# Optimization experiments

Measured on AMD Instinct MI355X. Metric: run time of the kernel, lower is better.

Reference implementation:

```python
import jax, jax.numpy as jnp
import numpy as np

DIM = 768      # embedding dim
NH = 12        # num heads
HD = DIM // NH # head dim = 64
WIN = 14       # window size
MLP = 4 * DIM  # mlp hidden
EPS = 1e-5     # torch LayerNorm default


def _layernorm(x, g, b):
    m = x.mean(-1, keepdims=True)
    v = ((x - m) ** 2).mean(-1, keepdims=True)
    return (x - m) * jax.lax.rsqrt(v + EPS) * g + b


def setup_inputs() -> dict:
    key = jax.random.key(0)
    ks = jax.random.split(key, 8)
    def n(k, shape, s=0.02):
        return jax.random.normal(k, shape, dtype=jnp.float32) * s
    return dict(
        x=jax.random.normal(ks[0], (2, 64, 64, DIM), dtype=jnp.float32),
        g1=jnp.ones((DIM,), jnp.float32), b1=jnp.zeros((DIM,), jnp.float32),
        w_qkv=n(ks[1], (DIM, 3 * DIM)), b_qkv=jnp.zeros((3 * DIM,), jnp.float32),
        w_proj=n(ks[2], (DIM, DIM)), b_proj=jnp.zeros((DIM,), jnp.float32),
        rel_h=n(ks[3], (2 * WIN - 1, HD)), rel_w=n(ks[4], (2 * WIN - 1, HD)),
        g2=jnp.ones((DIM,), jnp.float32), b2=jnp.zeros((DIM,), jnp.float32),
        w1=n(ks[5], (DIM, MLP)), b1_mlp=jnp.zeros((MLP,), jnp.float32),
        w2=n(ks[6], (MLP, DIM)), b2_mlp=jnp.zeros((DIM,), jnp.float32),
    )


def reference(x, g1, b1, w_qkv, b_qkv, w_proj, b_proj, rel_h, rel_w,
              g2, b2, w1, b1_mlp, w2, b2_mlp):
    B, H, W, C = x.shape
    shortcut = x
    xn = _layernorm(x, g1, b1)

    # ---- window partition with zero padding (H,W -> Hp,Wp) ----
    pad_h = (-H) % WIN
    pad_w = (-W) % WIN
    xp = jnp.pad(xn, ((0, 0), (0, pad_h), (0, pad_w), (0, 0)))
    Hp, Wp = H + pad_h, W + pad_w
    nwh, nww = Hp // WIN, Wp // WIN
    wins = xp.reshape(B, nwh, WIN, nww, WIN, C).transpose(0, 1, 3, 2, 4, 5)
    wins = wins.reshape(B * nwh * nww, WIN, WIN, C)
    Nw = wins.shape[0]
    HW = WIN * WIN

    # ---- attention (q/k size == window size; no rel-pos interpolation) ----
    qkv = (wins.reshape(Nw, HW, C) @ w_qkv + b_qkv).reshape(Nw, HW, 3, NH, HD)
    q, k, v = jnp.moveaxis(qkv, 2, 0)           # each [Nw, HW, NH, HD]
    q = q.transpose(0, 2, 1, 3)                  # [Nw, NH, HW, HD]
    k = k.transpose(0, 2, 1, 3)
    v = v.transpose(0, 2, 1, 3)
    scale = HD ** -0.5
    attn = jnp.einsum('nhqd,nhkd->nhqk', q * scale, k)  # [Nw, NH, HW, HW]

    # decomposed relative position bias
    idx = jnp.arange(WIN)[:, None] - jnp.arange(WIN)[None, :] + (WIN - 1)
    Rh = rel_h[idx]
    Rw = rel_w[idx]
    qr = q.reshape(Nw, NH, WIN, WIN, HD)
    bh = jnp.einsum('nihwd,hkd->nihwk', qr, Rh)  # bias over key-h
    bw = jnp.einsum('nihwd,wkd->nihwk', qr, Rw)  # bias over key-w
    attn = attn.reshape(Nw, NH, WIN, WIN, WIN, WIN)
    attn = attn + bh[..., :, None] + bw[..., None, :]
    attn = jax.nn.softmax(attn.reshape(Nw, NH, HW, HW), axis=-1)

    out = jnp.einsum('nhqk,nhkd->nhqd', attn, v)          # [Nw, NH, HW, HD]
    out = out.transpose(0, 2, 1, 3).reshape(Nw, WIN, WIN, C)
    out = out @ w_proj + b_proj

    # ---- window unpartition + crop padding ----
    out = out.reshape(B, nwh, nww, WIN, WIN, C).transpose(0, 1, 3, 2, 4, 5)
    out = out.reshape(B, Hp, Wp, C)[:, :H, :W, :]

    x = shortcut + out
    xn2 = _layernorm(x, g2, b2)
    mlp = jax.nn.gelu(xn2 @ w1 + b1_mlp, approximate=False) @ w2 + b2_mlp
    return x + mlp
```

## Files before the change

kernel.cpp:

```cpp
#include <hip/hip_runtime.h>
#include <cstdint>

#define CDIM 768
#define NHEAD 12
#define HD 64
#define WSZ 14
#define HW 196
#define NWIN 50
#define MWINP 9856
#define MTOK 8192
#define MLPD 3072

typedef unsigned short u16;
typedef short s16x8 __attribute__((ext_vector_type(8)));
typedef float f32x4 __attribute__((ext_vector_type(4)));

__device__ __forceinline__ float bf2f(u16 u) {
  union { uint32_t i; float f; } v; v.i = ((uint32_t)u) << 16; return v.f;
}
__device__ __forceinline__ u16 f2bf(float f) {
  union { float f; uint32_t i; } v; v.f = f;
  uint32_t u = v.i;
  return (u16)((u + 0x7FFFu + ((u >> 16) & 1u)) >> 16);
}

__global__ __launch_bounds__(256) void k_transpose(const float* __restrict__ W,
                                                   u16* __restrict__ WT, int K, int N) {
  __shared__ float tile[32][33];
  const int tx = threadIdx.x & 31, ty = threadIdx.x >> 5;
  const int bn = blockIdx.x * 32, bk = blockIdx.y * 32;
#pragma unroll
  for (int r = 0; r < 4; ++r)
    tile[ty + r * 8][tx] = W[(size_t)(bk + ty + r * 8) * N + bn + tx];
  __syncthreads();
#pragma unroll
  for (int r = 0; r < 4; ++r)
    WT[(size_t)(bn + ty + r * 8) * K + bk + tx] = f2bf(tile[tx][ty + r * 8]);
}

__global__ __launch_bounds__(256) void k_ln1(const float* __restrict__ x, const float* __restrict__ g,
                                             const float* __restrict__ b, u16* __restrict__ xnwin) {
  const int row = blockIdx.x * 4 + (threadIdx.x >> 6);
  const int lane = threadIdx.x & 63;
  const int win = row / HW, p = row % HW;
  bool valid = win < NWIN;
  int tok = 0;
  if (valid) {
    int bw = win / 25, rem = win % 25;
    int wr = rem / 5, wc = rem % 5;
    int i = p / WSZ, j = p % WSZ;
    int hh = wr * WSZ + i, ww = wc * WSZ + j;
    valid = (hh < 64) && (ww < 64);
    tok = (bw * 64 + hh) * 64 + ww;
  }
  u16* orow = xnwin + (size_t)row * CDIM;
  if (!valid) {
    ushort4 z; z.x = z.y = z.z = z.w = 0;
#pragma unroll
    for (int c = 0; c < 3; ++c) ((ushort4*)orow)[c * 64 + lane] = z;
    return;
  }
  const float4* xr = (const float4*)(x + (size_t)tok * CDIM);
  float4 v[3];
  float s = 0.f, sq = 0.f;
#pragma unroll
  for (int c = 0; c < 3; ++c) {
    v[c] = xr[c * 64 + lane];
    s += v[c].x + v[c].y + v[c].z + v[c].w;
    sq += v[c].x * v[c].x + v[c].y * v[c].y + v[c].z * v[c].z + v[c].w * v[c].w;
  }
#pragma unroll
  for (int off = 32; off > 0; off >>= 1) { s += __shfl_xor(s, off); sq += __shfl_xor(sq, off); }
  const float mean = s * (1.f / CDIM);
  const float rstd = rsqrtf(sq * (1.f / CDIM) - mean * mean + 1e-5f);
#pragma unroll
  for (int c = 0; c < 3; ++c) {
    float4 gv = ((const float4*)g)[c * 64 + lane];
    float4 bv = ((const float4*)b)[c * 64 + lane];
    ushort4 o;
    o.x = f2bf((v[c].x - mean) * rstd * gv.x + bv.x);
    o.y = f2bf((v[c].y - mean) * rstd * gv.y + bv.y);
    o.z = f2bf((v[c].z - mean) * rstd * gv.z + bv.z);
    o.w = f2bf((v[c].w - mean) * rstd * gv.w + bv.w);
    ((ushort4*)orow)[c * 64 + lane] = o;
  }
}

__global__ __launch_bounds__(256) void k_ln2(const float* __restrict__ xin, const float* __restrict__ g,
                                             const float* __restrict__ b, u16* __restrict__ xn2) {
  const int row = blockIdx.x * 4 + (threadIdx.x >> 6);
  const int lane = threadIdx.x & 63;
  const float4* xr = (const float4*)(xin + (size_t)row * CDIM);
  float4 v[3];
  float s = 0.f, sq = 0.f;
#pragma unroll
  for (int c = 0; c < 3; ++c) {
    v[c] = xr[c * 64 + lane];
    s += v[c].x + v[c].y + v[c].z + v[c].w;
    sq += v[c].x * v[c].x + v[c].y * v[c].y + v[c].z * v[c].z + v[c].w * v[c].w;
  }
#pragma unroll
  for (int off = 32; off > 0; off >>= 1) { s += __shfl_xor(s, off); sq += __shfl_xor(sq, off); }
  const float mean = s * (1.f / CDIM);
  const float rstd = rsqrtf(sq * (1.f / CDIM) - mean * mean + 1e-5f);
  u16* orow = xn2 + (size_t)row * CDIM;
#pragma unroll
  for (int c = 0; c < 3; ++c) {
    float4 gv = ((const float4*)g)[c * 64 + lane];
    float4 bv = ((const float4*)b)[c * 64 + lane];
    ushort4 o;
    o.x = f2bf((v[c].x - mean) * rstd * gv.x + bv.x);
    o.y = f2bf((v[c].y - mean) * rstd * gv.y + bv.y);
    o.z = f2bf((v[c].z - mean) * rstd * gv.z + bv.z);
    o.w = f2bf((v[c].w - mean) * rstd * gv.w + bv.w);
    ((ushort4*)orow)[c * 64 + lane] = o;
  }
}

template <int EPI>
__global__ __launch_bounds__(256) void k_gemm(const u16* __restrict__ A, const u16* __restrict__ BT,
                                              const float* __restrict__ bias, void* __restrict__ outp,
                                              const float* __restrict__ resid, int M, int N, int K) {
  __shared__ __align__(16) char lds[16384];
  char* ldsA = lds;
  char* ldsB = lds + 8192;
  const int t = threadIdx.x;
  const int lane = t & 63, wav = t >> 6;
  const int wm = wav >> 1, wn = wav & 1;
  const int lr = lane & 15, lg = lane >> 4;
  const int m0 = blockIdx.y * 128, n0 = blockIdx.x * 128;
  const int sr = t & 127, sg = t >> 7;

  const u16* gA0 = A + (size_t)(m0 + sr) * K + sg * 8;
  const u16* gA1 = gA0 + 16;
  const u16* gB0 = BT + (size_t)(n0 + sr) * K + sg * 8;
  const u16* gB1 = gB0 + 16;
  char* lA0 = ldsA + t * 16;
  char* lA1 = lA0 + 4096;
  char* lB0 = ldsB + t * 16;
  char* lB1 = lB0 + 4096;

  const char* pa = ldsA + (lg * 128 + wm * 64 + lr) * 16;
  const char* pb = ldsB + (lg * 128 + wn * 64 + lr) * 16;

  f32x4 acc[4][4];
#pragma unroll
  for (int i = 0; i < 4; ++i)
#pragma unroll
    for (int j = 0; j < 4; ++j) { acc[i][j][0] = 0.f; acc[i][j][1] = 0.f; acc[i][j][2] = 0.f; acc[i][j][3] = 0.f; }

  uint4 ra0 = *(const uint4*)gA0, ra1 = *(const uint4*)gA1;
  uint4 rb0 = *(const uint4*)gB0, rb1 = *(const uint4*)gB1;

  const int KT = K >> 5;
  for (int kt = 0; kt < KT; ++kt) {
    __syncthreads();
    *(uint4*)lA0 = ra0; *(uint4*)lA1 = ra1;
    *(uint4*)lB0 = rb0; *(uint4*)lB1 = rb1;
    __syncthreads();
    if (kt + 1 < KT) {
      gA0 += 32; gA1 += 32; gB0 += 32; gB1 += 32;
      ra0 = *(const uint4*)gA0; ra1 = *(const uint4*)gA1;
      rb0 = *(const uint4*)gB0; rb1 = *(const uint4*)gB1;
    }
    s16x8 av[4], bv[4];
#pragma unroll
    for (int i = 0; i < 4; ++i) av[i] = *(const s16x8*)(pa + i * 256);
#pragma unroll
    for (int j = 0; j < 4; ++j) bv[j] = *(const s16x8*)(pb + j * 256);
#pragma unroll
    for (int i = 0; i < 4; ++i)
#pragma unroll
      for (int j = 0; j < 4; ++j)
        acc[i][j] = __builtin_amdgcn_mfma_f32_16x16x32_bf16(av[i], bv[j], acc[i][j], 0, 0, 0);
  }

#pragma unroll
  for (int i = 0; i < 4; ++i) {
#pragma unroll
    for (int j = 0; j < 4; ++j) {
      const int gcol = n0 + wn * 64 + j * 16 + lr;
      const float bc = bias[gcol];
#pragma unroll
      for (int r = 0; r < 4; ++r) {
        const int grow = m0 + wm * 64 + i * 16 + lg * 4 + r;
        const float cv = acc[i][j][r] + bc;
        if constexpr (EPI == 0) {
          ((u16*)outp)[(size_t)grow * N + gcol] = f2bf(cv);
        } else if constexpr (EPI == 1) {
          const int winI = grow / HW, p = grow % HW;
          if (winI < NWIN) {
            const int bw = winI / 25, rem = winI % 25;
            const int wr = rem / 5, wc = rem % 5;
            const int i2 = p / WSZ, j2 = p % WSZ;
            const int hh = wr * WSZ + i2, ww = wc * WSZ + j2;
            if (hh < 64 && ww < 64) {
              const size_t tok = (size_t)(bw * 64 + hh) * 64 + ww;
              ((float*)outp)[tok * CDIM + gcol] = resid[tok * CDIM + gcol] + cv;
            }
          }
        } else if constexpr (EPI == 2) {
          const float gel = 0.5f * cv * (1.f + erff(cv * 0.70710678118654752f));
          ((u16*)outp)[(size_t)grow * N + gcol] = f2bf(gel);
        } else {
          ((float*)outp)[(size_t)grow * N + gcol] += cv;
        }
      }
    }
  }
}

__global__ __launch_bounds__(256) void k_relbias(const u16* __restrict__ qkv, const float* __restrict__ rel_h,
                                                 const float* __restrict__ rel_w, float* __restrict__ biasbuf) {
  const int idx = blockIdx.x * 256 + threadIdx.x;
  if (idx >= NWIN * NHEAD * HW * 28) return;
  const int c = idx % 28;
  const int p = (idx / 28) % HW;
  const int wh = idx / (28 * HW);
  const int win = wh / NHEAD, head = wh % NHEAD;
  const int i = p / WSZ, j = p % WSZ;
  const float* tbl = (c < 14) ? (rel_h + (size_t)(i - c + 13) * HD)
                              : (rel_w + (size_t)(j - (c - 14) + 13) * HD);
  const u16* q = qkv + ((size_t)win * HW + p) * 2304 + head * HD;
  float acc = 0.f;
#pragma unroll 8
  for (int d = 0; d < HD; ++d) acc += bf2f(q[d]) * tbl[d];
  biasbuf[idx] = acc;
}

__global__ __launch_bounds__(256) void k_attn(const u16* __restrict__ qkv, const float* __restrict__ biasbuf,
                                              u16* __restrict__ attnout) {
  __shared__ __align__(16) char lds[114112];
  char* Kl = lds;
  char* Vt = lds + 26624;
  char* Pb = lds + 59392;
  float* Bl = (float*)(lds + 92160);

  const int wh = blockIdx.x;
  const int win = wh / NHEAD, head = wh % NHEAD;
  const int t = threadIdx.x, lane = t & 63, w = t >> 6;
  const int lr = lane & 15, lg = lane >> 4;
  const size_t rowbase = (size_t)win * HW;
  const u16* qbase = qkv + rowbase * 2304 + head * HD;

  for (int i = t; i < 208 * 8; i += 256) {
    const int key = i >> 3, c = i & 7;
    uint4 v; v.x = v.y = v.z = v.w = 0u;
    if (key < HW) v = *(const uint4*)(qbase + (size_t)key * 2304 + 768 + c * 8);
    *(uint4*)(Kl + key * 128 + ((c ^ (key & 7)) << 4)) = v;
  }
  for (int i = t; i < 224 * 8; i += 256) {
    const int key = i >> 3, c8 = i & 7;
    uint4 v; v.x = v.y = v.z = v.w = 0u;
    if (key < HW) v = *(const uint4*)(qbase + (size_t)key * 2304 + 1536 + c8 * 8);
    const uint32_t vv[4] = {v.x, v.y, v.z, v.w};
    const int cc = key >> 3, grp = (cc >> 3) << 7, sub = cc & 7, ko = (key & 7) * 2;
#pragma unroll
    for (int e = 0; e < 4; ++e) {
      const int d0 = c8 * 8 + 2 * e;
      *(u16*)(Vt + d0 * 512 + grp + ((sub ^ (d0 & 7)) << 4) + ko) = (u16)(vv[e] & 0xffffu);
      const int d1 = d0 + 1;
      *(u16*)(Vt + d1 * 512 + grp + ((sub ^ (d1 & 7)) << 4) + ko) = (u16)(vv[e] >> 16);
    }
  }
  {
    const float* bsrc = biasbuf + (size_t)wh * (HW * 28);
    for (int i = t; i < HW * 28; i += 256) Bl[i] = bsrc[i];
  }
  {
    char* P = Pb + w * 8192;
    for (int i = lane; i < 16 * 6; i += 64) {
      const int row = i / 6, cc = 26 + i % 6;
      uint4 z; z.x = z.y = z.z = z.w = 0u;
      *(uint4*)(P + row * 512 + ((cc >> 3) << 7) + (((cc & 7) ^ (row & 7)) << 4)) = z;
    }
  }
  __syncthreads();

  char* P = Pb + w * 8192;
  for (int qt = w; qt < 13; qt += 4) {
    const int q0 = qt * 16;
    const s16x8 qa0 = *(const s16x8*)(qbase + (size_t)(q0 + lr) * 2304 + lg * 8);
    const s16x8 qa1 = *(const s16x8*)(qbase + (size_t)(q0 + lr) * 2304 + 32 + lg * 8);

    f32x4 st[13];
#pragma unroll
    for (int kt = 0; kt < 13; ++kt) {
      const int key = kt * 16 + lr;
      const s16x8 kb0 = *(const s16x8*)(Kl + key * 128 + ((lg ^ (key & 7)) << 4));
      const s16x8 kb1 = *(const s16x8*)(Kl + key * 128 + (((4 + lg) ^ (key & 7)) << 4));
      f32x4 z; z[0] = 0.f; z[1] = 0.f; z[2] = 0.f; z[3] = 0.f;
      z = __builtin_amdgcn_mfma_f32_16x16x32_bf16(qa0, kb0, z, 0, 0, 0);
      z = __builtin_amdgcn_mfma_f32_16x16x32_bf16(qa1, kb1, z, 0, 0, 0);
      st[kt] = z;
    }

    float mx[4] = {-1e30f, -1e30f, -1e30f, -1e30f};
#pragma unroll
    for (int r = 0; r < 4; ++r) {
      const int q = q0 + 4 * lg + r;
      const float* bq = Bl + (q < HW ? q : HW - 1) * 28;
#pragma unroll
      for (int kt = 0; kt < 13; ++kt) {
        float v;
        if (kt == 12 && lr >= 4) {
          v = -1e30f;
        } else {
          const int key = kt * 16 + lr;
          const int kh = key / 14, kw = key - kh * 14;
          v = st[kt][r] * 0.125f + bq[kh] + bq[14 + kw];
        }
        st[kt][r] = v;
        mx[r] = fmaxf(mx[r], v);
      }
    }
#pragma unroll
    for (int r = 0; r < 4; ++r)
#pragma unroll
      for (int off = 1; off < 16; off <<= 1) mx[r] = fmaxf(mx[r], __shfl_xor(mx[r], off));

    float sum[4] = {0.f, 0.f, 0.f, 0.f};
#pragma unroll
    for (int kt = 0; kt < 13; ++kt)
#pragma unroll
      for (int r = 0; r < 4; ++r) {
        const float e = __expf(st[kt][r] - mx[r]);
        st[kt][r] = e;
        sum[r] += e;
      }
    float inv[4];
#pragma unroll
    for (int r = 0; r < 4; ++r) {
#pragma unroll
      for (int off = 1; off < 16; off <<= 1) sum[r] += __shfl_xor(sum[r], off);
      inv[r] = 1.f / sum[r];
    }

#pragma unroll
    for (int r = 0; r < 4; ++r) {
      const int row = 4 * lg + r;
#pragma unroll
      for (int kt = 0; kt < 13; ++kt) {
        const int col = kt * 16 + lr;
        const int cc = col >> 3;
        *(u16*)(P + row * 512 + ((cc >> 3) << 7) + (((cc & 7) ^ (row & 7)) << 4) + (col & 7) * 2)
            = f2bf(st[kt][r] * inv[r]);
      }
    }

#pragma unroll
    for (int dt = 0; dt < 4; ++dt) {
      const int drow = dt * 16 + lr;
      f32x4 oz; oz[0] = 0.f; oz[1] = 0.f; oz[2] = 0.f; oz[3] = 0.f;
#pragma unroll
      for (int kb = 0; kb < 7; ++kb) {
        const int c = kb * 4 + lg;
        const int go = (c >> 3) << 7, sb = c & 7;
        const s16x8 pa = *(const s16x8*)(P + lr * 512 + go + ((sb ^ (lr & 7)) << 4));
        const s16x8 vb = *(const s16x8*)(Vt + drow * 512 + go + ((sb ^ (drow & 7)) << 4));
        oz = __builtin_amdgcn_mfma_f32_16x16x32_bf16(pa, vb, oz, 0, 0, 0);
      }
#pragma unroll
      for (int r = 0; r < 4; ++r) {
        const int q = q0 + 4 * lg + r;
        if (q < HW)
          attnout[(rowbase + q) * (size_t)CDIM + head * HD + drow] = f2bf(oz[r]);
      }
    }
  }
}

extern "C" void kernel_launch(void* const* d_in, const int* in_sizes, int n_in,
                              void* d_out, int out_size, void* d_ws, size_t ws_size,
                              hipStream_t stream) {
  const float* x     = (const float*)d_in[0];
  const float* g1    = (const float*)d_in[1];
  const float* b1    = (const float*)d_in[2];
  const float* w_qkv = (const float*)d_in[3];
  const float* b_qkv = (const float*)d_in[4];
  const float* w_proj= (const float*)d_in[5];
  const float* b_proj= (const float*)d_in[6];
  const float* rel_h = (const float*)d_in[7];
  const float* rel_w = (const float*)d_in[8];
  const float* g2    = (const float*)d_in[9];
  const float* b2    = (const float*)d_in[10];
  const float* w1    = (const float*)d_in[11];
  const float* b1m   = (const float*)d_in[12];
  const float* w2    = (const float*)d_in[13];
  const float* b2m   = (const float*)d_in[14];
  float* out = (float*)d_out;
  char* ws = (char*)d_ws;

  u16* wqkvT   = (u16*)(ws + 0);
  u16* wprojT  = (u16*)(ws + 3538944);
  u16* w1T     = (u16*)(ws + 4718592);
  u16* w2T     = (u16*)(ws + 9437184);
  u16* xnwin   = (u16*)(ws + 14155776);
  u16* qkv     = (u16*)(ws + 29294592);
  u16* attnout = (u16*)(ws + 79626240);
  float* biasbuf = (float*)(ws + 94765056);

  k_transpose<<<dim3(2304 / 32, 768 / 32), 256, 0, stream>>>(w_qkv, wqkvT, 768, 2304);
  k_transpose<<<dim3(768 / 32, 768 / 32), 256, 0, stream>>>(w_proj, wprojT, 768, 768);
  k_transpose<<<dim3(3072 / 32, 768 / 32), 256, 0, stream>>>(w1, w1T, 768, 3072);
  k_transpose<<<dim3(768 / 32, 3072 / 32), 256, 0, stream>>>(w2, w2T, 3072, 768);

  k_ln1<<<MWINP / 4, 256, 0, stream>>>(x, g1, b1, xnwin);

  k_gemm<0><<<dim3(2304 / 128, MWINP / 128), 256, 0, stream>>>(xnwin, wqkvT, b_qkv, qkv, nullptr, MWINP, 2304, 768);

  k_relbias<<<(NWIN * NHEAD * HW * 28 + 255) / 256, 256, 0, stream>>>(qkv, rel_h, rel_w, biasbuf);

  k_attn<<<NWIN * NHEAD, 256, 0, stream>>>(qkv, biasbuf, attnout);

  k_gemm<1><<<dim3(768 / 128, MWINP / 128), 256, 0, stream>>>(attnout, wprojT, b_proj, out, x, MWINP, 768, 768);

  k_ln2<<<MTOK / 4, 256, 0, stream>>>(out, g2, b2, xnwin );

  k_gemm<2><<<dim3(3072 / 128, MTOK / 128), 256, 0, stream>>>(xnwin, w1T, b1m, qkv , nullptr, MTOK, 3072, 768);

  k_gemm<3><<<dim3(768 / 128, MTOK / 128), 256, 0, stream>>>(qkv , w2T, b2m, out, nullptr, MTOK, 768, 3072);
}
```

Baseline: 659.6 us.

## Use direct global-to-LDS loads with triple-buffered pipeline in GEMM

Replaces the register-staged global loads and LDS stores in the bf16 MFMA GEMM with global_load_lds instructions that write straight into LDS. Uses a three-stage ring buffer with explicit vmcnt waits and one barrier per k-step, keeping two tiles in flight. The aim is to hide global memory latency and drop the second barrier and the register round-trip. LDS use rises from 16KB to 48KB per block, which may reduce occupancy. The per-wave 1024-byte offset must match the layout the MFMA fragment reads expect.

```diff
diff --git a/kernel.cpp b/kernel.cpp
--- a/kernel.cpp
+++ b/kernel.cpp
@@ -22,6 +22,11 @@
   union { float f; uint32_t i; } v; v.f = f;
   uint32_t u = v.i;
   return (u16)((u + 0x7FFFu + ((u >> 16) & 1u)) >> 16);
+}
+
+__device__ __forceinline__ void gld16(const u16* g, char* l) {
+  __builtin_amdgcn_global_load_lds((const __attribute__((address_space(1))) uint32_t*)g,
+                                   (__attribute__((address_space(3))) uint32_t*)l, 16, 0, 0);
 }
 
 __global__ __launch_bounds__(256) void k_transpose(const float* __restrict__ W,
@@ -121,27 +126,27 @@
 __global__ __launch_bounds__(256) void k_gemm(const u16* __restrict__ A, const u16* __restrict__ BT,
                                               const float* __restrict__ bias, void* __restrict__ outp,
                                               const float* __restrict__ resid, int M, int N, int K) {
-  __shared__ __align__(16) char lds[16384];
-  char* ldsA = lds;
-  char* ldsB = lds + 8192;
+  __shared__ __align__(16) char lds[49152];
   const int t = threadIdx.x;
   const int lane = t & 63, wav = t >> 6;
   const int wm = wav >> 1, wn = wav & 1;
   const int lr = lane & 15, lg = lane >> 4;
   const int m0 = blockIdx.y * 128, n0 = blockIdx.x * 128;
   const int sr = t & 127, sg = t >> 7;
-
-  const u16* gA0 = A + (size_t)(m0 + sr) * K + sg * 8;
-  const u16* gA1 = gA0 + 16;
-  const u16* gB0 = BT + (size_t)(n0 + sr) * K + sg * 8;
-  const u16* gB1 = gB0 + 16;
-  char* lA0 = ldsA + t * 16;
-  char* lA1 = lA0 + 4096;
-  char* lB0 = ldsB + t * 16;
-  char* lB1 = lB0 + 4096;
-
-  const char* pa = ldsA + (lg * 128 + wm * 64 + lr) * 16;
-  const char* pb = ldsB + (lg * 128 + wn * 64 + lr) * 16;
+  const int wofs = wav * 1024;
+
+  const u16* arow = A + (size_t)(m0 + sr) * K + sg * 8;
+  const u16* brow = BT + (size_t)(n0 + sr) * K + sg * 8;
+
+#define STAGE(base, kt)                                   \
+  do {                                                    \
+    const u16* a0_ = arow + (kt) * 32;                    \
+    const u16* b0_ = brow + (kt) * 32;                    \
+    gld16(a0_,      (base) + wofs);                       \
+    gld16(a0_ + 16, (base) + 4096 + wofs);                \
+    gld16(b0_,      (base) + 8192 + wofs);                \
+    gld16(b0_ + 16, (base) + 12288 + wofs);               \
+  } while (0)
 
   f32x4 acc[4][4];
 #pragma unroll
@@ -149,31 +154,38 @@
 #pragma unroll
     for (int j = 0; j < 4; ++j) { acc[i][j][0] = 0.f; acc[i][j][1] = 0.f; acc[i][j][2] = 0.f; acc[i][j][3] = 0.f; }
 
-  uint4 ra0 = *(const uint4*)gA0, ra1 = *(const uint4*)gA1;
-  uint4 rb0 = *(const uint4*)gB0, rb1 = *(const uint4*)gB1;
-
+  char* p0 = lds;
+  char* p1 = lds + 16384;
+  char* p2 = lds + 32768;
   const int KT = K >> 5;
+
+  STAGE(p0, 0);
+  STAGE(p1, 1);
+
+  const int aofs = (lg * 128 + wm * 64 + lr) * 16;
+  const int bofs = 8192 + (lg * 128 + wn * 64 + lr) * 16;
+
   for (int kt = 0; kt < KT; ++kt) {
-    __syncthreads();
-    *(uint4*)lA0 = ra0; *(uint4*)lA1 = ra1;
-    *(uint4*)lB0 = rb0; *(uint4*)lB1 = rb1;
-    __syncthreads();
-    if (kt + 1 < KT) {
-      gA0 += 32; gA1 += 32; gB0 += 32; gB1 += 32;
-      ra0 = *(const uint4*)gA0; ra1 = *(const uint4*)gA1;
-      rb0 = *(const uint4*)gB0; rb1 = *(const uint4*)gB1;
-    }
+    if (kt < KT - 1) asm volatile("s_waitcnt vmcnt(4)" ::: "memory");
+    else             asm volatile("s_waitcnt vmcnt(0)" ::: "memory");
+    asm volatile("s_waitcnt lgkmcnt(0)" ::: "memory");
+    __builtin_amdgcn_s_barrier();
+    if (kt + 2 < KT) STAGE(p2, kt + 2);
+
     s16x8 av[4], bv[4];
 #pragma unroll
-    for (int i = 0; i < 4; ++i) av[i] = *(const s16x8*)(pa + i * 256);
-#pragma unroll
-    for (int j = 0; j < 4; ++j) bv[j] = *(const s16x8*)(pb + j * 256);
+    for (int i = 0; i < 4; ++i) av[i] = *(const s16x8*)(p0 + aofs + i * 256);
+#pragma unroll
+    for (int j = 0; j < 4; ++j) bv[j] = *(const s16x8*)(p0 + bofs + j * 256);
 #pragma unroll
     for (int i = 0; i < 4; ++i)
 #pragma unroll
       for (int j = 0; j < 4; ++j)
         acc[i][j] = __builtin_amdgcn_mfma_f32_16x16x32_bf16(av[i], bv[j], acc[i][j], 0, 0, 0);
-  }
+
+    char* tmp = p0; p0 = p1; p1 = p2; p2 = tmp;
+  }
+#undef STAGE
 
 #pragma unroll
   for (int i = 0; i < 4; ++i) {
```

Measured after the change: 665.5 us. Within noise of the previous version (+0.9%).
